# Optimization experiments

Hardware: AMD Instinct MI355X
Metric: run time of the kernel (lower is better)

The kernel has to match this reference:

```python
import jax, jax.numpy as jnp
import numpy as np

HIDDEN = 128
N_HID = 7            # hidden_layers - 1 internal GELU blocks
N_TERMS = 2          # number of separable terms per side
N_IN = 1             # vars per term
B = 16384
STEP_SIZE = 0.1
NUM_STEPS = 1

# Forest-Ruth 4th-order symplectic coefficients
_K = 2.0 ** (1.0 / 3.0)
_C = (1.0 / (2.0 * (2.0 - _K)), (1.0 - _K) / (2.0 * (2.0 - _K)),
      (1.0 - _K) / (2.0 * (2.0 - _K)), 1.0 / (2.0 * (2.0 - _K)))
_D = (1.0 / (2.0 - _K), -_K / (2.0 - _K), 1.0 / (2.0 - _K), 0.0)


def _mlp(W0, b0, Wh, bh, Wo, bo, x):
    # x: [B, n_in] -> [B, 1]; torch GELU default is exact (erf)
    h = jax.nn.gelu(x @ W0 + b0, approximate=False)
    for i in range(N_HID):
        h = jax.nn.gelu(h @ Wh[i] + bh[i], approximate=False)
    return h @ Wo + bo


def _side_scalar(W0, b0, Wh, bh, Wo, bo, idx, x):
    # gather per-term feature subsets, run all term-MLPs batched via vmap,
    # sum over terms and batch (GradientWrapper takes grad of the summed scalar)
    xs = jnp.moveaxis(x[:, idx], 1, 0)            # [n_terms, B, n_in]
    outs = jax.vmap(_mlp)(W0, b0, Wh, bh, Wo, bo, xs)  # [n_terms, B, 1]
    return outs.sum()


def setup_inputs() -> dict:
    key = jax.random.key(0)
    ks = jax.random.split(key, 3)
    s = 0.05

    def pset(k):
        kk = jax.random.split(k, 6)
        return (
            jax.random.normal(kk[0], (N_TERMS, N_IN, HIDDEN), jnp.float32) * s,
            jax.random.normal(kk[1], (N_TERMS, HIDDEN), jnp.float32) * s,
            jax.random.normal(kk[2], (N_TERMS, N_HID, HIDDEN, HIDDEN), jnp.float32) * s,
            jax.random.normal(kk[3], (N_TERMS, N_HID, HIDDEN), jnp.float32) * s,
            jax.random.normal(kk[4], (N_TERMS, HIDDEN, 1), jnp.float32) * s,
            jax.random.normal(kk[5], (N_TERMS, 1), jnp.float32) * s,
        )

    lW0, lb0, lWh, lbh, lWo, lbo = pset(ks[0])
    rW0, rb0, rWh, rbh, rWo, rbo = pset(ks[1])
    X = jax.random.normal(ks[2], (B, 4), jnp.float32)
    left_idx = jnp.arange(N_TERMS, dtype=jnp.int32).reshape(N_TERMS, N_IN)
    right_idx = jnp.arange(N_TERMS, dtype=jnp.int32).reshape(N_TERMS, N_IN)
    return dict(X=X, lW0=lW0, lb0=lb0, lWh=lWh, lbh=lbh, lWo=lWo, lbo=lbo,
                rW0=rW0, rb0=rb0, rWh=rWh, rbh=rbh, rWo=rWo, rbo=rbo,
                left_idx=left_idx, right_idx=right_idx)


def reference(X, lW0, lb0, lWh, lbh, lWo, lbo,
              rW0, rb0, rWh, rbh, rWo, rbo, left_idx, right_idx):
    # H(q, p) = V(q) + T(p); left side = V(q), right side = T(p)
    dVdq = jax.grad(lambda q: _side_scalar(lW0, lb0, lWh, lbh, lWo, lbo, left_idx, q))
    dTdp = jax.grad(lambda p: _side_scalar(rW0, rb0, rWh, rbh, rWo, rbo, right_idx, p))
    dt = jnp.float32(STEP_SIZE)
    nq = X.shape[1] // 2
    q = X[:, :nq]
    p = X[:, nq:]
    for _ in range(NUM_STEPS):
        for c, d in zip(_C, _D):
            q = q + jnp.float32(c) * dt * dTdp(p)   # dq/dt =  dH/dp
            p = p - jnp.float32(d) * dt * dVdq(q)   # dp/dt = -dH/dq
    return jnp.concatenate((q, p), axis=1)
```

## Files before the change

kernel.cpp:

```cpp
#include <hip/hip_runtime.h>

#define NLAYER 7
#define IMGB 16384
#define WSCALE 16.0f

typedef __attribute__((ext_vector_type(2))) float float2v;
typedef __attribute__((ext_vector_type(4))) float float4v;
typedef unsigned long long u64;

__device__ __forceinline__ float2v pk_fma(float2v a, float2v b, float2v c){
  return __builtin_elementwise_fma(a, b, c);
}
__device__ __forceinline__ float2v lo2(float4v v){ return (float2v){v[0], v[1]}; }
__device__ __forceinline__ float2v hi2(float4v v){ return (float2v){v[2], v[3]}; }

__device__ __forceinline__ unsigned pk4fp8(float v0, float v1, float v2, float v3){
  int w = __builtin_amdgcn_cvt_pk_fp8_f32(v0, v1, 0, false);
  w = __builtin_amdgcn_cvt_pk_fp8_f32(v2, v3, w, true);
  return (unsigned)w;
}
template<bool HI>
__device__ __forceinline__ float2v up2(unsigned w){
  return __builtin_amdgcn_cvt_pk_f32_fp8((int)w, HI);
}
__device__ __forceinline__ float4v mfma8(u64 a, u64 b, float4v c){
  return __builtin_amdgcn_mfma_f32_16x16x32_fp8_fp8((long)a, (long)b, c, 0, 0, 0);
}
__device__ __forceinline__ void act2(float2v z, float2v& P16, float2v& gp16){
  const float2v c1v  = {6.3830764862829235f, 6.3830764862829235f};
  const float2v c3v  = {-1.0638460810704874f, -1.0638460810704874f};
  const float2v c33v = {-3.1915382432114624f, -3.1915382432114624f};
  const float2v v8   = {8.f, 8.f};
  float2v z2 = z * z;
  float2v u  = pk_fma(z2, c3v, c1v);
  P16 = pk_fma(z, u, v8);
  float2v Pd = pk_fma(z2, c33v, c1v);
  gp16 = pk_fma(z, Pd, P16);
}

__device__ __forceinline__ void gl2lds16(const unsigned char* g, unsigned char* l){
  __builtin_amdgcn_global_load_lds((const __attribute__((address_space(1))) unsigned int*)g,
                                   (__attribute__((address_space(3))) unsigned int*)l,
                                   16, 0, 0);
}

__global__ void prep_weights(const float* __restrict__ lWh,
                             const float* __restrict__ rWh,
                             unsigned* __restrict__ wbf)
{
  int idx = blockIdx.x * 256 + threadIdx.x;
  if (idx >= 4*NLAYER*IMGB/4) return;
  int j0 = (idx & 1) * 4;
  int cs = (idx >> 1) & 15;
  int n  = (idx >> 5) & 127;
  int rem = idx >> 12;
  int L   = rem % NLAYER;
  int net = rem / NLAYER;
  int side = net >> 1, term = net & 1;
  int kb = ((cs ^ (n & 15)) << 3) + j0;
  const float* src = side ? rWh : lWh;
  const float* base = src + (size_t)((term*NLAYER + L)*128)*128 + n;
  float v0 = base[(kb+0)*128] * WSCALE;
  float v1 = base[(kb+1)*128] * WSCALE;
  float v2 = base[(kb+2)*128] * WSCALE;
  float v3 = base[(kb+3)*128] * WSCALE;
  wbf[idx] = pk4fp8(v0, v1, v2, v3);
}

__global__ __launch_bounds__(256, 4)
void sympl_main(const float* __restrict__ X,
                const float* __restrict__ lW0, const float* __restrict__ lb0,
                const float* __restrict__ lbh, const float* __restrict__ lWo,
                const float* __restrict__ rW0, const float* __restrict__ rb0,
                const float* __restrict__ rbh, const float* __restrict__ rWo,
                const int* __restrict__ lidx, const int* __restrict__ ridx,
                const unsigned char* __restrict__ wbf,
                float* __restrict__ out)
{
  __shared__ __align__(16) unsigned char sW[IMGB];
  __shared__ __align__(16) unsigned char sH[8192];

  const int tid  = threadIdx.x;
  const int lane = tid & 63;
  const int w    = tid >> 6;
  const int m0   = lane & 15;
  const int q    = lane >> 4;
  const int g    = w & 1;
  const int ih   = w >> 1;
  const int col  = blockIdx.y;
  const int e0   = blockIdx.x * 32;
  const int r    = tid >> 3;
  const int sg   = tid & 7;
  const int rs   = r & 15;

  const int lt = (lidx[0] == col) ? 0 : 1;
  const int rt = (ridx[0] == col) ? 0 : 1;

  float qv = X[(e0 + r)*4 + col];
  float pv = X[(e0 + r)*4 + 2 + col];

  const float dt = 0.1f;
  const float C0 = 0.6756035959798289f, C1 = -0.17560359597982883f;
  const float D0 = 1.3512071919596578f, D1 = -1.7024143839193153f;
  const float is = 1.0f / 262144.0f;
  const float coefs[7] = { C0*dt*is, -D0*dt*is, C1*dt*is, -D1*dt*is,
                           C1*dt*is, -D0*dt*is, C0*dt*is };

  const float2v inv256v = {1.f/256.f, 1.f/256.f};
  const float2v inv64v  = {1.f/64.f, 1.f/64.f};

  {
    const unsigned char* src = wbf + (size_t)(2 + rt)*NLAYER*IMGB;
    #pragma unroll
    for (int it = 0; it < 4; ++it){
      int o = (it*256 + tid) * 16;
      gl2lds16(src + o, sW + o);
    }
  }
  __syncthreads();

  for (int ev = 0; ev < 7; ++ev){
    const bool isT = !(ev & 1);
    const int  term = isT ? rt : lt;
    const float* W0p = (isT ? rW0 : lW0) + term*128;
    const float* b0p = (isT ? rb0 : lb0) + term*128;
    const float* bhp = (isT ? rbh : lbh) + term*NLAYER*128;
    const float* Wop = (isT ? rWo : lWo) + term*128;
    const unsigned char* wimg = wbf + (size_t)(((isT ? 2 : 0) + term)*NLAYER)*IMGB;
    const int tnx = (ev & 1) ? rt : lt;
    const unsigned char* wimg_nx = wbf + (size_t)((((ev & 1) ? 2 : 0) + tnx)*NLAYER)*IMGB;

    {
      const float x = isT ? pv : qv;
      const float2v xv = {x, x};
      unsigned char* pH = sH + r*128;
      unsigned char* pD = pH + 32*128;
      #pragma unroll
      for (int c = 0; c < 2; ++c){
        int n0 = sg*16 + c*8;
        float4v wa = *(const float4v*)(W0p + n0);
        float4v wb = *(const float4v*)(W0p + n0 + 4);
        float4v ba = *(const float4v*)(b0p + n0);
        float4v bb = *(const float4v*)(b0p + n0 + 4);
        float2v zp[4] = { pk_fma(xv, lo2(wa), lo2(ba)), pk_fma(xv, hi2(wa), hi2(ba)),
                          pk_fma(xv, lo2(wb), lo2(bb)), pk_fma(xv, hi2(wb), hi2(bb)) };
        float2v wp[4] = { lo2(wa), hi2(wa), lo2(wb), hi2(wb) };
        float Sh[8], Sd[8];
        #pragma unroll
        for (int pp = 0; pp < 4; ++pp){
          float2v P16, gp16; act2(zp[pp], P16, gp16);
          float2v h = zp[pp] * P16;
          float2v d = gp16 * wp[pp];
          Sh[pp*2] = h[0]; Sh[pp*2+1] = h[1];
          Sd[pp*2] = d[0]; Sd[pp*2+1] = d[1];
        }
        u64 hv = (u64)pk4fp8(Sh[0],Sh[1],Sh[2],Sh[3]) | ((u64)pk4fp8(Sh[4],Sh[5],Sh[6],Sh[7]) << 32);
        u64 dv = (u64)pk4fp8(Sd[0],Sd[1],Sd[2],Sd[3]) | ((u64)pk4fp8(Sd[4],Sd[5],Sd[6],Sd[7]) << 32);
        int off = ((2*sg + c) ^ rs) * 8;
        *(u64*)(pH + off) = hv;
        *(u64*)(pD + off) = dv;
      }
    }
    __syncthreads();

    const unsigned char* pB0 = sH + (g*16 + m0)*128;
    const unsigned char* pB1 = pB0 + 32*128;
    const unsigned char* pA  = sW + (ih*64 + m0)*128;
    unsigned char* pHe = sH + (g*16 + m0)*128;
    unsigned char* pDe = pHe + 32*128;

    for (int L = 0; L < NLAYER; ++L){
      float4v acc[4][2];
      #pragma unroll
      for (int i = 0; i < 4; ++i){
        acc[i][0] = (float4v){0.f,0.f,0.f,0.f};
        acc[i][1] = (float4v){0.f,0.f,0.f,0.f};
      }
      #pragma unroll
      for (int ks = 0; ks < 4; ++ks){
        const int co = ((ks*4 + q) ^ m0) * 8;
        u64 b0 = *(const u64*)(pB0 + co);
        u64 b1 = *(const u64*)(pB1 + co);
        #pragma unroll
        for (int i = 0; i < 4; ++i){
          u64 a = *(const u64*)(pA + i*2048 + co);
          acc[i][0] = mfma8(a, b0, acc[i][0]);
          acc[i][1] = mfma8(a, b1, acc[i][1]);
        }
      }
      __syncthreads();

      if (!(ev == 6 && L == 6)){
        const unsigned char* nsrc = (L < 6) ? (wimg + (size_t)(L+1)*IMGB) : wimg_nx;
        #pragma unroll
        for (int it = 0; it < 4; ++it){
          int o = (it*256 + tid) * 16;
          gl2lds16(nsrc + o, sW + o);
        }
      }

      const float* bias = bhp + L*128;
      const bool last = (L == NLAYER-1);
      #pragma unroll
      for (int i = 0; i < 4; ++i){
        const int I = ih*4 + i;
        float4v bv = *(const float4v*)(bias + I*16 + q*4);
        float2v za = pk_fma(lo2(acc[i][0]), inv256v, lo2(bv));
        float2v zb = pk_fma(hi2(acc[i][0]), inv256v, hi2(bv));
        float2v ta = lo2(acc[i][1]) * inv64v;
        float2v tb = hi2(acc[i][1]) * inv64v;
        float2v Pa, ga, Pb, gb;
        act2(za, Pa, ga);
        act2(zb, Pb, gb);
        float2v ha = za * Pa, hb = zb * Pb;
        float2v da = ga * ta, db = gb * tb;
        const int off = ((I*2 + (q >> 1)) ^ m0) * 8 + (q & 1) * 4;
        if (!last) *(unsigned*)(pHe + off) = pk4fp8(ha[0], ha[1], hb[0], hb[1]);
        *(unsigned*)(pDe + off) = pk4fp8(da[0], da[1], db[0], db[1]);
      }
      __syncthreads();
    }

    {
      const unsigned char* pD = sH + (32 + r)*128;
      float2v sv = {0.f, 0.f};
      #pragma unroll
      for (int c = 0; c < 2; ++c){
        u64 dv8 = *(const u64*)(pD + ((2*sg + c) ^ rs) * 8);
        unsigned wlo = (unsigned)dv8, whi = (unsigned)(dv8 >> 32);
        float4v woa = *(const float4v*)(Wop + sg*16 + c*8);
        float4v wob = *(const float4v*)(Wop + sg*16 + c*8 + 4);
        sv = pk_fma(up2<false>(wlo), lo2(woa), sv);
        sv = pk_fma(up2<true>(wlo),  hi2(woa), sv);
        sv = pk_fma(up2<false>(whi), lo2(wob), sv);
        sv = pk_fma(up2<true>(whi),  hi2(wob), sv);
      }
      float s = sv[0] + sv[1];
      s += __shfl_xor(s, 1);
      s += __shfl_xor(s, 2);
      s += __shfl_xor(s, 4);
      if (isT) qv += coefs[ev] * s;
      else     pv += coefs[ev] * s;
    }
    __syncthreads();
  }

  if (sg == 0){
    out[(e0 + r)*4 + col]     = qv;
    out[(e0 + r)*4 + 2 + col] = pv;
  }
}

extern "C" void kernel_launch(void* const* d_in, const int* in_sizes, int n_in,
                              void* d_out, int out_size, void* d_ws, size_t ws_size,
                              hipStream_t stream)
{
  const float* X   = (const float*)d_in[0];
  const float* lW0 = (const float*)d_in[1];
  const float* lb0 = (const float*)d_in[2];
  const float* lWh = (const float*)d_in[3];
  const float* lbh = (const float*)d_in[4];
  const float* lWo = (const float*)d_in[5];
  const float* rW0 = (const float*)d_in[7];
  const float* rb0 = (const float*)d_in[8];
  const float* rWh = (const float*)d_in[9];
  const float* rbh = (const float*)d_in[10];
  const float* rWo = (const float*)d_in[11];
  const int*   li  = (const int*)d_in[13];
  const int*   ri  = (const int*)d_in[14];
  unsigned char* wbf = (unsigned char*)d_ws;
  float* out = (float*)d_out;
  const int B = in_sizes[0] / 4;

  const int words = 4 * NLAYER * IMGB / 4;
  hipLaunchKernelGGL(prep_weights, dim3((words + 255)/256), dim3(256), 0, stream,
                     lWh, rWh, (unsigned*)wbf);
  hipLaunchKernelGGL(sympl_main, dim3(B/32, 2), dim3(256), 0, stream,
                     X, lW0, lb0, lbh, lWo, rW0, rb0, rbh, rWo, li, ri, wbf, out);
}
```

Measured before the change: 208.7 us.

## Load fp8 weight fragments into registers and double-buffer activation LDS

The main kernel no longer stages each layer's weight image through LDS. Each lane loads its own A-fragments straight from global memory into registers, and the next layer's fragments are prefetched during the epilogue. Activations are double-buffered across two LDS halves, which removes one barrier per layer and one per evaluation, and the epilogue folds the scale factors into rescaled polynomial coefficients. The weight prep kernel now transposes through LDS with coalesced loads and a simple row-major layout without the XOR swizzle, at the cost of 16 extra registers per thread for the fragments and uncoalesced 8-byte global loads.

```diff
diff --git a/kernel.cpp b/kernel.cpp
--- a/kernel.cpp
+++ b/kernel.cpp
@@ -6,6 +6,7 @@
 
 typedef __attribute__((ext_vector_type(2))) float float2v;
 typedef __attribute__((ext_vector_type(4))) float float4v;
+typedef __attribute__((ext_vector_type(4))) unsigned int uint4v;
 typedef unsigned long long u64;
 
 __device__ __forceinline__ float2v pk_fma(float2v a, float2v b, float2v c){
@@ -38,33 +39,47 @@
   gp16 = pk_fma(z, Pd, P16);
 }
 
-__device__ __forceinline__ void gl2lds16(const unsigned char* g, unsigned char* l){
-  __builtin_amdgcn_global_load_lds((const __attribute__((address_space(1))) unsigned int*)g,
-                                   (__attribute__((address_space(3))) unsigned int*)l,
-                                   16, 0, 0);
-}
-
-__global__ void prep_weights(const float* __restrict__ lWh,
-                             const float* __restrict__ rWh,
-                             unsigned* __restrict__ wbf)
+__global__ __launch_bounds__(256)
+void prep_weights(const float* __restrict__ lWh,
+                  const float* __restrict__ rWh,
+                  unsigned char* __restrict__ wbf)
 {
-  int idx = blockIdx.x * 256 + threadIdx.x;
-  if (idx >= 4*NLAYER*IMGB/4) return;
-  int j0 = (idx & 1) * 4;
-  int cs = (idx >> 1) & 15;
-  int n  = (idx >> 5) & 127;
-  int rem = idx >> 12;
-  int L   = rem % NLAYER;
-  int net = rem / NLAYER;
-  int side = net >> 1, term = net & 1;
-  int kb = ((cs ^ (n & 15)) << 3) + j0;
-  const float* src = side ? rWh : lWh;
-  const float* base = src + (size_t)((term*NLAYER + L)*128)*128 + n;
-  float v0 = base[(kb+0)*128] * WSCALE;
-  float v1 = base[(kb+1)*128] * WSCALE;
-  float v2 = base[(kb+2)*128] * WSCALE;
-  float v3 = base[(kb+3)*128] * WSCALE;
-  wbf[idx] = pk4fp8(v0, v1, v2, v3);
+  __shared__ __align__(16) unsigned char T[IMGB];
+  const int b = blockIdx.x;
+  const int net = b / NLAYER, L = b % NLAYER;
+  const int side = net >> 1, term = net & 1;
+  const float* src = (side ? rWh : lWh) + (size_t)((term*NLAYER + L)*128)*128;
+  const int t = threadIdx.x;
+  {
+    const int k = t >> 1, n0 = (t & 1)*64;
+    const float* row = src + k*128 + n0;
+    #pragma unroll
+    for (int c4 = 0; c4 < 4; ++c4){
+      float4v f0 = *(const float4v*)(row + c4*16);
+      float4v f1 = *(const float4v*)(row + c4*16 + 4);
+      float4v f2 = *(const float4v*)(row + c4*16 + 8);
+      float4v f3 = *(const float4v*)(row + c4*16 + 12);
+      uint4v wv = { pk4fp8(f0[0]*WSCALE, f0[1]*WSCALE, f0[2]*WSCALE, f0[3]*WSCALE),
+                    pk4fp8(f1[0]*WSCALE, f1[1]*WSCALE, f1[2]*WSCALE, f1[3]*WSCALE),
+                    pk4fp8(f2[0]*WSCALE, f2[1]*WSCALE, f2[2]*WSCALE, f2[3]*WSCALE),
+                    pk4fp8(f3[0]*WSCALE, f3[1]*WSCALE, f3[2]*WSCALE, f3[3]*WSCALE) };
+      *(uint4v*)&T[k*128 + n0 + c4*16] = wv;
+    }
+  }
+  __syncthreads();
+  {
+    const int n = t >> 1, c0 = (t & 1)*8;
+    unsigned char* dst = wbf + ((size_t)b << 14) + n*128;
+    #pragma unroll
+    for (int c = 0; c < 8; ++c){
+      const int kc = (c0 + c)*8;
+      u64 v = 0;
+      #pragma unroll
+      for (int j = 0; j < 8; ++j)
+        v |= (u64)T[(kc + j)*128 + n] << (8*j);
+      *(u64*)(dst + (c0 + c)*8) = v;
+    }
+  }
 }
 
 __global__ __launch_bounds__(256, 4)
@@ -77,8 +92,7 @@
                 const unsigned char* __restrict__ wbf,
                 float* __restrict__ out)
 {
-  __shared__ __align__(16) unsigned char sW[IMGB];
-  __shared__ __align__(16) unsigned char sH[8192];
+  __shared__ __align__(16) unsigned char sH[2][8192];
 
   const int tid  = threadIdx.x;
   const int lane = tid & 63;
@@ -92,6 +106,7 @@
   const int r    = tid >> 3;
   const int sg   = tid & 7;
   const int rs   = r & 15;
+  const int voff = (ih*64 + m0)*128 + q*8;
 
   const int lt = (lidx[0] == col) ? 0 : 1;
   const int rt = (ridx[0] == col) ? 0 : 1;
@@ -106,18 +121,23 @@
   const float coefs[7] = { C0*dt*is, -D0*dt*is, C1*dt*is, -D1*dt*is,
                            C1*dt*is, -D0*dt*is, C0*dt*is };
 
-  const float2v inv256v = {1.f/256.f, 1.f/256.f};
-  const float2v inv64v  = {1.f/64.f, 1.f/64.f};
-
+  const float2v v256 = {256.f, 256.f};
+  const float2v K0 = {0.03125f, 0.03125f};
+  const float2v K1 = {9.739801768e-5f, 9.739801768e-5f};
+  const float2v K3 = {-2.476767495e-10f, -2.476767495e-10f};
+  const float2v G0 = {0.125f, 0.125f};
+  const float2v G1 = {7.791841414e-4f, 7.791841414e-4f};
+  const float2v G3 = {-3.962875977e-9f, -3.962875977e-9f};
+
+  u64 a[4][4];
   {
-    const unsigned char* src = wbf + (size_t)(2 + rt)*NLAYER*IMGB;
+    const unsigned char* img = wbf + (size_t)(2 + rt)*NLAYER*IMGB;
     #pragma unroll
-    for (int it = 0; it < 4; ++it){
-      int o = (it*256 + tid) * 16;
-      gl2lds16(src + o, sW + o);
-    }
-  }
-  __syncthreads();
+    for (int i = 0; i < 4; ++i)
+      #pragma unroll
+      for (int ks = 0; ks < 4; ++ks)
+        a[i][ks] = *(const u64*)(img + voff + i*2048 + ks*32);
+  }
 
   for (int ev = 0; ev < 7; ++ev){
     const bool isT = !(ev & 1);
@@ -133,8 +153,8 @@
     {
       const float x = isT ? pv : qv;
       const float2v xv = {x, x};
-      unsigned char* pH = sH + r*128;
-      unsigned char* pD = pH + 32*128;
+      unsigned char* pH = sH[0] + r*128;
+      unsigned char* pD = pH + 4096;
       #pragma unroll
       for (int c = 0; c < 2; ++c){
         int n0 = sg*16 + c*8;
@@ -163,13 +183,10 @@
     }
     __syncthreads();
 
-    const unsigned char* pB0 = sH + (g*16 + m0)*128;
-    const unsigned char* pB1 = pB0 + 32*128;
-    const unsigned char* pA  = sW + (ih*64 + m0)*128;
-    unsigned char* pHe = sH + (g*16 + m0)*128;
-    unsigned char* pDe = pHe + 32*128;
-
     for (int L = 0; L < NLAYER; ++L){
+      const unsigned char* pB0 = sH[L & 1] + (g*16 + m0)*128;
+      const unsigned char* pB1 = pB0 + 4096;
+
       float4v acc[4][2];
       #pragma unroll
       for (int i = 0; i < 4; ++i){
@@ -183,46 +200,48 @@
         u64 b1 = *(const u64*)(pB1 + co);
         #pragma unroll
         for (int i = 0; i < 4; ++i){
-          u64 a = *(const u64*)(pA + i*2048 + co);
-          acc[i][0] = mfma8(a, b0, acc[i][0]);
-          acc[i][1] = mfma8(a, b1, acc[i][1]);
+          acc[i][0] = mfma8(a[i][ks], b0, acc[i][0]);
+          acc[i][1] = mfma8(a[i][ks], b1, acc[i][1]);
         }
       }
-      __syncthreads();
 
       if (!(ev == 6 && L == 6)){
-        const unsigned char* nsrc = (L < 6) ? (wimg + (size_t)(L+1)*IMGB) : wimg_nx;
+        const unsigned char* nimg = (L < 6) ? (wimg + (size_t)(L+1)*IMGB) : wimg_nx;
         #pragma unroll
-        for (int it = 0; it < 4; ++it){
-          int o = (it*256 + tid) * 16;
-          gl2lds16(nsrc + o, sW + o);
-        }
-      }
-
+        for (int i = 0; i < 4; ++i)
+          #pragma unroll
+          for (int ks = 0; ks < 4; ++ks)
+            a[i][ks] = *(const u64*)(nimg + voff + i*2048 + ks*32);
+      }
+
+      unsigned char* pHe = sH[(L+1) & 1] + (g*16 + m0)*128;
+      unsigned char* pDe = pHe + 4096;
       const float* bias = bhp + L*128;
       const bool last = (L == NLAYER-1);
       #pragma unroll
       for (int i = 0; i < 4; ++i){
         const int I = ih*4 + i;
         float4v bv = *(const float4v*)(bias + I*16 + q*4);
-        float2v za = pk_fma(lo2(acc[i][0]), inv256v, lo2(bv));
-        float2v zb = pk_fma(hi2(acc[i][0]), inv256v, hi2(bv));
-        float2v ta = lo2(acc[i][1]) * inv64v;
-        float2v tb = hi2(acc[i][1]) * inv64v;
-        float2v Pa, ga, Pb, gb;
-        act2(za, Pa, ga);
-        act2(zb, Pb, gb);
-        float2v ha = za * Pa, hb = zb * Pb;
-        float2v da = ga * ta, db = gb * tb;
+        float2v ua = pk_fma(lo2(bv), v256, lo2(acc[i][0]));
+        float2v ub = pk_fma(hi2(bv), v256, hi2(acc[i][0]));
+        float2v u2a = ua * ua, u2b = ub * ub;
+        float2v ga = pk_fma(ua, pk_fma(u2a, G3, G1), G0);
+        float2v gb = pk_fma(ub, pk_fma(u2b, G3, G1), G0);
+        float2v da = ga * lo2(acc[i][1]);
+        float2v db = gb * hi2(acc[i][1]);
         const int off = ((I*2 + (q >> 1)) ^ m0) * 8 + (q & 1) * 4;
-        if (!last) *(unsigned*)(pHe + off) = pk4fp8(ha[0], ha[1], hb[0], hb[1]);
+        if (!last){
+          float2v ha = ua * pk_fma(ua, pk_fma(u2a, K3, K1), K0);
+          float2v hb = ub * pk_fma(ub, pk_fma(u2b, K3, K1), K0);
+          *(unsigned*)(pHe + off) = pk4fp8(ha[0], ha[1], hb[0], hb[1]);
+        }
         *(unsigned*)(pDe + off) = pk4fp8(da[0], da[1], db[0], db[1]);
       }
       __syncthreads();
     }
 
     {
-      const unsigned char* pD = sH + (32 + r)*128;
+      const unsigned char* pD = sH[1] + 4096 + r*128;
       float2v sv = {0.f, 0.f};
       #pragma unroll
       for (int c = 0; c < 2; ++c){
@@ -242,7 +261,6 @@
       if (isT) qv += coefs[ev] * s;
       else     pv += coefs[ev] * s;
     }
-    __syncthreads();
   }
 
   if (sg == 0){
@@ -272,9 +290,8 @@
   float* out = (float*)d_out;
   const int B = in_sizes[0] / 4;
 
-  const int words = 4 * NLAYER * IMGB / 4;
-  hipLaunchKernelGGL(prep_weights, dim3((words + 255)/256), dim3(256), 0, stream,
-                     lWh, rWh, (unsigned*)wbf);
+  hipLaunchKernelGGL(prep_weights, dim3(4*NLAYER), dim3(256), 0, stream,
+                     lWh, rWh, wbf);
   hipLaunchKernelGGL(sympl_main, dim3(B/32, 2), dim3(256), 0, stream,
                      X, lW0, lb0, lbh, lWo, rW0, rb0, rbh, rWo, li, ri, wbf, out);
 }
```

After: 473.1 us. +126.7%, slower.
